# Optimization experiments

Hardware: AMD Instinct MI355X
Metric: run time of the kernel (lower is better)

Reference implementation:

```python
import jax, jax.numpy as jnp
import numpy as np

B = 131072
SD, AD, HID = 24, 8, 32
NH = SD + AD            # n_heads = 32
UNITS = HID * NH        # 1024


def _xavier(k, shape):
    fan_in, fan_out = shape[-2], shape[-1]
    lim = float(np.sqrt(6.0 / (fan_in + fan_out)))
    return jax.random.uniform(k, shape, jnp.float32, -lim, lim)


def setup_inputs() -> dict:
    key = jax.random.key(0)
    ks = jax.random.split(key, 8)
    return dict(
        state=jax.random.normal(ks[0], (B, SD), jnp.float32),
        action=jax.random.normal(ks[1], (B, AD), jnp.float32),
        # ripple layer 1: per-head Linear(NH -> HID), gate logits init 0 (init_prob=0.5)
        W1=_xavier(ks[2], (NH, NH, HID)), b1=jnp.zeros((NH, HID), jnp.float32), g1=jnp.zeros((NH,), jnp.float32),
        # ripple layer 2: per-head Linear(UNITS -> HID)
        W2=_xavier(ks[3], (NH, UNITS, HID)), b2=jnp.zeros((NH, HID), jnp.float32), g2=jnp.zeros((NH,), jnp.float32),
        # q_network
        Wq1=_xavier(ks[4], (UNITS, 256)), bq1=jnp.zeros((256,), jnp.float32),
        ln1_g=jnp.ones((256,), jnp.float32), ln1_b=jnp.zeros((256,), jnp.float32),
        Wq2=_xavier(ks[5], (256, 128)), bq2=jnp.zeros((128,), jnp.float32),
        ln2_g=jnp.ones((128,), jnp.float32), ln2_b=jnp.zeros((128,), jnp.float32),
        Wq3=_xavier(ks[6], (128, 1)), bq3=jnp.zeros((1,), jnp.float32),
    )


def _ripple(x, W, b, g):
    # x: [B, D]; W: [H, D, K]; per-head linear + tanh, scaled by per-head sigmoid gate
    h = jnp.tanh(jnp.einsum('bd,hdk->bhk', x, W) + b[None])  # [B, H, K]
    h = h * jax.nn.sigmoid(g)[None, :, None]
    return h.reshape(x.shape[0], -1)  # [B, H*K]


def _ln(x, g, b, eps=1e-5):
    mu = jnp.mean(x, -1, keepdims=True)
    var = jnp.mean((x - mu) ** 2, -1, keepdims=True)
    return (x - mu) * jax.lax.rsqrt(var + eps) * g + b


def reference(state, action, W1, b1, g1, W2, b2, g2,
              Wq1, bq1, ln1_g, ln1_b, Wq2, bq2, ln2_g, ln2_b, Wq3, bq3):
    sa = jnp.concatenate([state, action], axis=1)          # [B, SD+AD]
    x = _ripple(sa, W1, b1, g1)                            # [B, UNITS]
    x = _ripple(x, W2, b2, g2)                             # [B, UNITS]
    h = jax.nn.relu(_ln(x @ Wq1 + bq1, ln1_g, ln1_b))      # [B, 256] (dropout = eval identity)
    h = jax.nn.relu(_ln(h @ Wq2 + bq2, ln2_g, ln2_b))      # [B, 128]
    return h @ Wq3 + bq3                                   # [B, 1]
```

## Files before the change

kernel.cpp:

```cpp
#include <hip/hip_runtime.h>
#include <hip/hip_bf16.h>

typedef _Float16 f16x8 __attribute__((ext_vector_type(8)));
typedef float f32x4 __attribute__((ext_vector_type(4)));

__device__ __forceinline__ void async16(const _Float16* g, _Float16* l) {
  __builtin_amdgcn_global_load_lds(
      (const __attribute__((address_space(1))) unsigned int*)g,
      (__attribute__((address_space(3))) unsigned int*)l, 16, 0, 0);
}

__device__ __forceinline__ float tanh_fast(float x) {
  float e = __expf(2.0f * x);
  return 1.0f - 2.0f * __builtin_amdgcn_rcpf(e + 1.0f);
}
__device__ __forceinline__ float sigmoid_fast(float x) {
  return __builtin_amdgcn_rcpf(1.0f + __expf(-x));
}

__global__ __launch_bounds__(256) void transpose_cvt(const float* __restrict__ in,
                                                     _Float16* __restrict__ out,
                                                     int R, int C) {
  __shared__ float tile[32][33];
  int z = blockIdx.z;
  in  += (size_t)z * R * C;
  out += (size_t)z * R * C;
  int r0 = blockIdx.x * 32, c0 = blockIdx.y * 32;
  int t = threadIdx.x;
  int cc = t & 31, rr8 = t >> 5;
#pragma unroll
  for (int p = 0; p < 4; ++p) {
    int r = rr8 + p * 8;
    tile[cc][r] = in[(size_t)(r0 + r) * C + c0 + cc];
  }
  __syncthreads();
  int rr = t & 31, cc8 = t >> 5;
#pragma unroll
  for (int p = 0; p < 4; ++p) {
    int c = cc8 + p * 8;
    out[(size_t)(c0 + c) * R + r0 + rr] = (_Float16)tile[c][rr];
  }
}

__global__ __launch_bounds__(256) void k1_ripple1(
    const float* __restrict__ state, const float* __restrict__ action,
    const _Float16* __restrict__ v1t, const float* __restrict__ b1,
    const float* __restrict__ g1, _Float16* __restrict__ x1, int gro) {
  __shared__ __align__(16) _Float16 As[128 * 40];
  int bn = blockIdx.x, bm = blockIdx.y;
  int t = threadIdx.x, w = t >> 6, l = t & 63, q = l >> 4, l15 = l & 15;
  int n0 = bn * 128, m0 = bm * 128;

  {
    int r = t >> 1, half = t & 1;
    size_t grow = (size_t)(gro + m0 + r);
    float v[16];
    if (half == 0) {
      const float4* sp = (const float4*)(state + grow * 24);
      ((float4*)v)[0] = sp[0]; ((float4*)v)[1] = sp[1];
      ((float4*)v)[2] = sp[2]; ((float4*)v)[3] = sp[3];
    } else {
      const float4* sp = (const float4*)(state + grow * 24 + 16);
      ((float4*)v)[0] = sp[0]; ((float4*)v)[1] = sp[1];
      const float4* ap = (const float4*)(action + grow * 8);
      ((float4*)v)[2] = ap[0]; ((float4*)v)[3] = ap[1];
    }
    f16x8 h0, h1;
#pragma unroll
    for (int j = 0; j < 8; ++j) { h0[j] = (_Float16)v[j]; h1[j] = (_Float16)v[8 + j]; }
    *(f16x8*)&As[r * 40 + half * 16] = h0;
    *(f16x8*)&As[r * 40 + half * 16 + 8] = h1;
  }
  __syncthreads();

  int wr = w >> 1, wc = w & 1;
  f16x8 af[4], bf[4];
#pragma unroll
  for (int mi = 0; mi < 4; ++mi)
    af[mi] = *(const f16x8*)&As[(wr * 64 + mi * 16 + l15) * 40 + q * 8];
#pragma unroll
  for (int ni = 0; ni < 4; ++ni)
    bf[ni] = *(const f16x8*)(v1t + (size_t)(n0 + wc * 64 + ni * 16 + l15) * 32 + q * 8);

  f32x4 acc[4][4] = {};
#pragma unroll
  for (int mi = 0; mi < 4; ++mi)
#pragma unroll
    for (int ni = 0; ni < 4; ++ni)
      acc[mi][ni] = __builtin_amdgcn_mfma_f32_16x16x32_f16(af[mi], bf[ni], acc[mi][ni], 0, 0, 0);

#pragma unroll
  for (int ni = 0; ni < 4; ++ni) {
    int col = n0 + wc * 64 + ni * 16 + l15;
    float sg = sigmoid_fast(g1[col >> 5]);
    float bias = b1[col];
#pragma unroll
    for (int mi = 0; mi < 4; ++mi)
#pragma unroll
      for (int r = 0; r < 4; ++r) {
        int row = m0 + wr * 64 + mi * 16 + q * 4 + r;
        x1[(size_t)row * 1024 + col] = (_Float16)(tanh_fast(acc[mi][ni][r] + bias) * sg);
      }
  }
}

__global__ __launch_bounds__(256, 3) void k2_ripple2(
    const _Float16* __restrict__ x1, const _Float16* __restrict__ v2t,
    const float* __restrict__ b2, const float* __restrict__ g2,
    _Float16* __restrict__ x2, int nbm) {
  __shared__ __align__(16) _Float16 As[128 * 32];
  __shared__ __align__(16) _Float16 Bs[128 * 32];
  int g = blockIdx.x;
  int bn, bm;
  if ((nbm & 7) == 0) {
    int x = g & 7, j = g >> 3;
    bn = j & 7; bm = x + 8 * (j >> 3);
  } else { bn = g & 7; bm = g >> 3; }
  int t = threadIdx.x, w = t >> 6, l = t & 63, q = l >> 4, l15 = l & 15;
  int n0 = bn * 128, m0 = bm * 128;
  int wr = w >> 1, wc = w & 1;
  f32x4 acc[4][4] = {};

  int c0 = t, c1 = t + 256;
  const _Float16* aS0 = x1 + (size_t)(m0 + (c0 >> 2)) * 1024 + ((c0 & 3) ^ ((c0 >> 3) & 3)) * 8;
  const _Float16* aS1 = x1 + (size_t)(m0 + (c1 >> 2)) * 1024 + ((c1 & 3) ^ ((c1 >> 3) & 3)) * 8;
  const _Float16* bS0 = v2t + (size_t)(n0 + (c0 >> 2)) * 1024 + ((c0 & 3) ^ ((c0 >> 3) & 3)) * 8;
  const _Float16* bS1 = v2t + (size_t)(n0 + (c1 >> 2)) * 1024 + ((c1 & 3) ^ ((c1 >> 3) & 3)) * 8;
  _Float16* aD0 = As + c0 * 8; _Float16* aD1 = As + c1 * 8;
  _Float16* bD0 = Bs + c0 * 8; _Float16* bD1 = Bs + c1 * 8;
  int qs = q ^ ((l15 >> 1) & 3);

  for (int kt = 0; kt < 32; ++kt) {
    __syncthreads();
    int ko = kt * 32;
    async16(aS0 + ko, aD0);
    async16(aS1 + ko, aD1);
    async16(bS0 + ko, bD0);
    async16(bS1 + ko, bD1);
    __builtin_amdgcn_s_waitcnt(0);
    __syncthreads();
    f16x8 af[4], bf[4];
#pragma unroll
    for (int mi = 0; mi < 4; ++mi)
      af[mi] = *(const f16x8*)&As[(wr * 64 + mi * 16 + l15) * 32 + qs * 8];
#pragma unroll
    for (int ni = 0; ni < 4; ++ni)
      bf[ni] = *(const f16x8*)&Bs[(wc * 64 + ni * 16 + l15) * 32 + qs * 8];
#pragma unroll
    for (int mi = 0; mi < 4; ++mi)
#pragma unroll
      for (int ni = 0; ni < 4; ++ni)
        acc[mi][ni] = __builtin_amdgcn_mfma_f32_16x16x32_f16(af[mi], bf[ni], acc[mi][ni], 0, 0, 0);
  }

#pragma unroll
  for (int ni = 0; ni < 4; ++ni) {
    int col = n0 + wc * 64 + ni * 16 + l15;
    float sg = sigmoid_fast(g2[col >> 5]);
    float bias = b2[col];
#pragma unroll
    for (int mi = 0; mi < 4; ++mi)
#pragma unroll
      for (int r = 0; r < 4; ++r) {
        int row = m0 + wr * 64 + mi * 16 + q * 4 + r;
        x2[(size_t)row * 1024 + col] = (_Float16)(tanh_fast(acc[mi][ni][r] + bias) * sg);
      }
  }
}

__global__ __launch_bounds__(256) void k3_head(
    const _Float16* __restrict__ x2, const _Float16* __restrict__ t1t,
    const _Float16* __restrict__ t2t,
    const float* __restrict__ bq1, const float* __restrict__ ln1g, const float* __restrict__ ln1b,
    const float* __restrict__ bq2, const float* __restrict__ ln2g, const float* __restrict__ ln2b,
    const float* __restrict__ wq3, const float* __restrict__ bq3,
    float* __restrict__ out) {
  __shared__ __align__(16) _Float16 Ast[2 * 64 * 32];
  __shared__ __align__(16) _Float16 Bst[2 * 256 * 32];
  __shared__ __align__(16) _Float16 y1h[64 * 264];
  __shared__ float redA[64 * 4], redB[64 * 4];
  __shared__ float meanv[64], rstdv[64];
  int bm = blockIdx.x;
  int t = threadIdx.x, w = t >> 6, l = t & 63, q = l >> 4, l15 = l & 15;
  int m0 = bm * 64;
  int qs = q ^ ((l15 >> 1) & 3);

  f32x4 acc[4][4] = {};
  int cA = t;
  const _Float16* aS = x2 + (size_t)(m0 + (cA >> 2)) * 1024 + ((cA & 3) ^ ((cA >> 3) & 3)) * 8;
  _Float16* aD = Ast + cA * 8;
  const _Float16* bS[4]; _Float16* bD[4];
#pragma unroll
  for (int i = 0; i < 4; ++i) {
    int c = t + i * 256;
    bS[i] = t1t + (size_t)(c >> 2) * 1024 + ((c & 3) ^ ((c >> 3) & 3)) * 8;
    bD[i] = Bst + c * 8;
  }

  for (int kt = 0; kt < 16; ++kt) {
    __syncthreads();
    int ko = kt * 64;
    async16(aS + ko, aD);
    async16(aS + ko + 32, aD + 64 * 32);
#pragma unroll
    for (int i = 0; i < 4; ++i) {
      async16(bS[i] + ko, bD[i]);
      async16(bS[i] + ko + 32, bD[i] + 256 * 32);
    }
    __builtin_amdgcn_s_waitcnt(0);
    __syncthreads();
#pragma unroll
    for (int s = 0; s < 2; ++s) {
      f16x8 af[4], bf[4];
#pragma unroll
      for (int mi = 0; mi < 4; ++mi)
        af[mi] = *(const f16x8*)&Ast[s * 2048 + (mi * 16 + l15) * 32 + qs * 8];
#pragma unroll
      for (int ni = 0; ni < 4; ++ni)
        bf[ni] = *(const f16x8*)&Bst[s * 8192 + (w * 64 + ni * 16 + l15) * 32 + qs * 8];
#pragma unroll
      for (int mi = 0; mi < 4; ++mi)
#pragma unroll
        for (int ni = 0; ni < 4; ++ni)
          acc[mi][ni] = __builtin_amdgcn_mfma_f32_16x16x32_f16(af[mi], bf[ni], acc[mi][ni], 0, 0, 0);
    }
  }

#pragma unroll
  for (int ni = 0; ni < 4; ++ni) {
    int col = w * 64 + ni * 16 + l15;
    float b = bq1[col];
#pragma unroll
    for (int mi = 0; mi < 4; ++mi)
#pragma unroll
      for (int r = 0; r < 4; ++r) acc[mi][ni][r] += b;
  }
#pragma unroll
  for (int mi = 0; mi < 4; ++mi)
#pragma unroll
    for (int r = 0; r < 4; ++r) {
      int row = mi * 16 + q * 4 + r;
      float s = 0.f, sq = 0.f;
#pragma unroll
      for (int ni = 0; ni < 4; ++ni) { float v = acc[mi][ni][r]; s += v; sq += v * v; }
#pragma unroll
      for (int off = 1; off < 16; off <<= 1) { s += __shfl_xor(s, off); sq += __shfl_xor(sq, off); }
      if (l15 == 0) { redA[row * 4 + w] = s; redB[row * 4 + w] = sq; }
    }
  __syncthreads();
  if (t < 64) {
    float s  = redA[t * 4] + redA[t * 4 + 1] + redA[t * 4 + 2] + redA[t * 4 + 3];
    float sq = redB[t * 4] + redB[t * 4 + 1] + redB[t * 4 + 2] + redB[t * 4 + 3];
    float mean = s * (1.0f / 256.0f);
    float var = sq * (1.0f / 256.0f) - mean * mean;
    meanv[t] = mean; rstdv[t] = rsqrtf(var + 1e-5f);
  }
  __syncthreads();
#pragma unroll
  for (int mi = 0; mi < 4; ++mi)
#pragma unroll
    for (int ni = 0; ni < 4; ++ni)
#pragma unroll
      for (int r = 0; r < 4; ++r) {
        int row = mi * 16 + q * 4 + r;
        int col = w * 64 + ni * 16 + l15;
        float y = (acc[mi][ni][r] - meanv[row]) * rstdv[row] * ln1g[col] + ln1b[col];
        y = fmaxf(y, 0.f);
        y1h[row * 264 + col] = (_Float16)y;
      }
  __syncthreads();

  int wr = w >> 1, wc = w & 1;
  f32x4 a2[2][4] = {};
  for (int kt = 0; kt < 8; ++kt) {
    f16x8 af2[2];
#pragma unroll
    for (int mi = 0; mi < 2; ++mi)
      af2[mi] = *(const f16x8*)&y1h[(wr * 32 + mi * 16 + l15) * 264 + kt * 32 + q * 8];
#pragma unroll
    for (int ni = 0; ni < 4; ++ni) {
      f16x8 bf = *(const f16x8*)(t2t + (size_t)(wc * 64 + ni * 16 + l15) * 256 + kt * 32 + q * 8);
#pragma unroll
      for (int mi = 0; mi < 2; ++mi)
        a2[mi][ni] = __builtin_amdgcn_mfma_f32_16x16x32_f16(af2[mi], bf, a2[mi][ni], 0, 0, 0);
    }
  }
#pragma unroll
  for (int ni = 0; ni < 4; ++ni) {
    int col = wc * 64 + ni * 16 + l15;
    float b = bq2[col];
#pragma unroll
    for (int mi = 0; mi < 2; ++mi)
#pragma unroll
      for (int r = 0; r < 4; ++r) a2[mi][ni][r] += b;
  }
  __syncthreads();
#pragma unroll
  for (int mi = 0; mi < 2; ++mi)
#pragma unroll
    for (int r = 0; r < 4; ++r) {
      int row = wr * 32 + mi * 16 + q * 4 + r;
      float s = 0.f, sq = 0.f;
#pragma unroll
      for (int ni = 0; ni < 4; ++ni) { float v = a2[mi][ni][r]; s += v; sq += v * v; }
#pragma unroll
      for (int off = 1; off < 16; off <<= 1) { s += __shfl_xor(s, off); sq += __shfl_xor(sq, off); }
      if (l15 == 0) { redA[row * 2 + wc] = s; redB[row * 2 + wc] = sq; }
    }
  __syncthreads();
  if (t < 64) {
    float s = redA[t * 2] + redA[t * 2 + 1];
    float sq = redB[t * 2] + redB[t * 2 + 1];
    float mean = s * (1.0f / 128.0f);
    float var = sq * (1.0f / 128.0f) - mean * mean;
    meanv[t] = mean; rstdv[t] = rsqrtf(var + 1e-5f);
  }
  __syncthreads();
#pragma unroll
  for (int mi = 0; mi < 2; ++mi)
#pragma unroll
    for (int r = 0; r < 4; ++r) {
      int row = wr * 32 + mi * 16 + q * 4 + r;
      float pr = 0.f;
#pragma unroll
      for (int ni = 0; ni < 4; ++ni) {
        int col = wc * 64 + ni * 16 + l15;
        float y = (a2[mi][ni][r] - meanv[row]) * rstdv[row] * ln2g[col] + ln2b[col];
        y = fmaxf(y, 0.f);
        pr += y * wq3[col];
      }
#pragma unroll
      for (int off = 1; off < 16; off <<= 1) pr += __shfl_xor(pr, off);
      if (l15 == 0) redA[row * 2 + wc] = pr;
    }
  __syncthreads();
  if (t < 64) out[m0 + t] = redA[t * 2] + redA[t * 2 + 1] + bq3[0];
}

extern "C" void kernel_launch(void* const* d_in, const int* in_sizes, int n_in,
                              void* d_out, int out_size, void* d_ws, size_t ws_size,
                              hipStream_t stream) {
  const float* state  = (const float*)d_in[0];
  const float* action = (const float*)d_in[1];
  const float* W1  = (const float*)d_in[2];
  const float* b1  = (const float*)d_in[3];
  const float* g1  = (const float*)d_in[4];
  const float* W2  = (const float*)d_in[5];
  const float* b2  = (const float*)d_in[6];
  const float* g2  = (const float*)d_in[7];
  const float* Wq1 = (const float*)d_in[8];
  const float* bq1 = (const float*)d_in[9];
  const float* ln1g = (const float*)d_in[10];
  const float* ln1b = (const float*)d_in[11];
  const float* Wq2 = (const float*)d_in[12];
  const float* bq2 = (const float*)d_in[13];
  const float* ln2g = (const float*)d_in[14];
  const float* ln2b = (const float*)d_in[15];
  const float* Wq3 = (const float*)d_in[16];
  const float* bq3 = (const float*)d_in[17];
  int B = in_sizes[0] / 24;

  char* ws = (char*)d_ws;
  _Float16* V1t = (_Float16*)(ws);
  _Float16* V2t = (_Float16*)(ws + 65536);
  _Float16* T1t = (_Float16*)(ws + 65536 + 2097152);
  _Float16* T2t = (_Float16*)(ws + 65536 + 2097152 + 524288);
  size_t woff = (65536 + 2097152 + 524288 + 65536 + 4095) & ~(size_t)4095;

  size_t avail = ws_size > woff ? ws_size - woff : 0;
  long rows = (long)(avail / 4096);
  if (rows > 32768) rows = 32768;
  rows &= ~127L;
  if (rows < 128) rows = 128;
  int S = (int)rows;
  _Float16* x1 = (_Float16*)(ws + woff);
  _Float16* x2 = x1 + (size_t)S * 1024;

  transpose_cvt<<<dim3(1, 1, 32), 256, 0, stream>>>(W1, V1t, 32, 32);
  transpose_cvt<<<dim3(32, 1, 32), 256, 0, stream>>>(W2, V2t, 1024, 32);
  transpose_cvt<<<dim3(32, 8, 1), 256, 0, stream>>>(Wq1, T1t, 1024, 256);
  transpose_cvt<<<dim3(8, 4, 1), 256, 0, stream>>>(Wq2, T2t, 256, 128);

  for (int r0 = 0; r0 < B; r0 += S) {
    int Sc = S < (B - r0) ? S : (B - r0);
    int nbm = Sc / 128;
    k1_ripple1<<<dim3(8, nbm), 256, 0, stream>>>(state, action, V1t, b1, g1, x1, r0);
    k2_ripple2<<<dim3(8 * nbm), 256, 0, stream>>>(x1, V2t, b2, g2, x2, nbm);
    k3_head<<<dim3(Sc / 64), 256, 0, stream>>>(x2, T1t, T2t, bq1, ln1g, ln1b,
                                               bq2, ln2g, ln2b, Wq3, bq3,
                                               (float*)d_out + r0);
  }
}
```

Baseline: 702.6 us.

## Stage epilogue stores via LDS, merge weight transposes, retile head kernel

Merges the four weight-transpose launches into one kernel. The ripple epilogues now stage results in shared memory so global stores become coalesced 16-byte writes instead of scattered half-precision stores. The head kernel moves to 512 threads and 128-row tiles with a single-stage K loop, which halves how often the Wq1 tile is reloaded per row. When the workspace allows, k2 outputs are grouped so k3 launches over two slices at once. The trade-off is more LDS barriers in the epilogues and higher register and occupancy pressure in k3.

```diff
diff --git a/kernel.cpp b/kernel.cpp
--- a/kernel.cpp
+++ b/kernel.cpp
@@ -18,14 +18,26 @@
   return __builtin_amdgcn_rcpf(1.0f + __expf(-x));
 }
 
-__global__ __launch_bounds__(256) void transpose_cvt(const float* __restrict__ in,
-                                                     _Float16* __restrict__ out,
-                                                     int R, int C) {
+__global__ __launch_bounds__(256) void transpose_all(
+    const float* __restrict__ W1, const float* __restrict__ W2,
+    const float* __restrict__ Wq1, const float* __restrict__ Wq2,
+    _Float16* __restrict__ V1t, _Float16* __restrict__ V2t,
+    _Float16* __restrict__ T1t, _Float16* __restrict__ T2t) {
   __shared__ float tile[32][33];
-  int z = blockIdx.z;
-  in  += (size_t)z * R * C;
-  out += (size_t)z * R * C;
-  int r0 = blockIdx.x * 32, c0 = blockIdx.y * 32;
+  int b = blockIdx.x;
+  const float* in; _Float16* out; int R, C, rt, ct;
+  if (b < 32) {
+    in = W1 + b * 1024; out = V1t + b * 1024; R = 32; C = 32; rt = 0; ct = 0;
+  } else if (b < 32 + 1024) {
+    int i = b - 32; int z = i >> 5;
+    in = W2 + (size_t)z * 32768; out = V2t + (size_t)z * 32768;
+    R = 1024; C = 32; rt = i & 31; ct = 0;
+  } else if (b < 32 + 1024 + 256) {
+    int i = b - 1056; in = Wq1; out = T1t; R = 1024; C = 256; rt = i >> 3; ct = i & 7;
+  } else {
+    int i = b - 1312; in = Wq2; out = T2t; R = 256; C = 128; rt = i >> 2; ct = i & 3;
+  }
+  int r0 = rt * 32, c0 = ct * 32;
   int t = threadIdx.x;
   int cc = t & 31, rr8 = t >> 5;
 #pragma unroll
@@ -89,27 +101,37 @@
     for (int ni = 0; ni < 4; ++ni)
       acc[mi][ni] = __builtin_amdgcn_mfma_f32_16x16x32_f16(af[mi], bf[ni], acc[mi][ni], 0, 0, 0);
 
-#pragma unroll
   for (int ni = 0; ni < 4; ++ni) {
+    __syncthreads();
     int col = n0 + wc * 64 + ni * 16 + l15;
     float sg = sigmoid_fast(g1[col >> 5]);
     float bias = b1[col];
+    int cl = wc * 16 + l15;
 #pragma unroll
     for (int mi = 0; mi < 4; ++mi)
 #pragma unroll
       for (int r = 0; r < 4; ++r) {
-        int row = m0 + wr * 64 + mi * 16 + q * 4 + r;
-        x1[(size_t)row * 1024 + col] = (_Float16)(tanh_fast(acc[mi][ni][r] + bias) * sg);
+        int rl = wr * 64 + mi * 16 + q * 4 + r;
+        As[rl * 40 + cl] = (_Float16)(tanh_fast(acc[mi][ni][r] + bias) * sg);
       }
-  }
-}
-
-__global__ __launch_bounds__(256, 3) void k2_ripple2(
+    __syncthreads();
+#pragma unroll
+    for (int i = 0; i < 2; ++i) {
+      int c = t + i * 256;
+      int row = c >> 2, sub = c & 3;
+      int colg = n0 + (sub >> 1) * 64 + ni * 16 + (sub & 1) * 8;
+      *(float4*)(x1 + (size_t)(m0 + row) * 1024 + colg) = *(const float4*)&As[row * 40 + sub * 8];
+    }
+  }
+}
+
+__global__ __launch_bounds__(256, 4) void k2_ripple2(
     const _Float16* __restrict__ x1, const _Float16* __restrict__ v2t,
     const float* __restrict__ b2, const float* __restrict__ g2,
     _Float16* __restrict__ x2, int nbm) {
-  __shared__ __align__(16) _Float16 As[128 * 32];
-  __shared__ __align__(16) _Float16 Bs[128 * 32];
+  __shared__ __align__(16) _Float16 SMEM[9216];
+  _Float16* As = SMEM;
+  _Float16* Bs = SMEM + 4096;
   int g = blockIdx.x;
   int bn, bm;
   if ((nbm & 7) == 0) {
@@ -153,82 +175,86 @@
         acc[mi][ni] = __builtin_amdgcn_mfma_f32_16x16x32_f16(af[mi], bf[ni], acc[mi][ni], 0, 0, 0);
   }
 
-#pragma unroll
-  for (int ni = 0; ni < 4; ++ni) {
-    int col = n0 + wc * 64 + ni * 16 + l15;
-    float sg = sigmoid_fast(g2[col >> 5]);
-    float bias = b2[col];
-#pragma unroll
-    for (int mi = 0; mi < 4; ++mi)
-#pragma unroll
-      for (int r = 0; r < 4; ++r) {
-        int row = m0 + wr * 64 + mi * 16 + q * 4 + r;
-        x2[(size_t)row * 1024 + col] = (_Float16)(tanh_fast(acc[mi][ni][r] + bias) * sg);
-      }
-  }
-}
-
-__global__ __launch_bounds__(256) void k3_head(
+  for (int pass = 0; pass < 2; ++pass) {
+    __syncthreads();
+#pragma unroll
+    for (int ni2 = 0; ni2 < 2; ++ni2) {
+      int ni = pass * 2 + ni2;
+      int col = n0 + wc * 64 + ni * 16 + l15;
+      float sg = sigmoid_fast(g2[col >> 5]);
+      float bias = b2[col];
+      int cl = wc * 32 + ni2 * 16 + l15;
+#pragma unroll
+      for (int mi = 0; mi < 4; ++mi)
+#pragma unroll
+        for (int r = 0; r < 4; ++r) {
+          int rl = wr * 64 + mi * 16 + q * 4 + r;
+          SMEM[rl * 72 + cl] = (_Float16)(tanh_fast(acc[mi][ni][r] + bias) * sg);
+        }
+    }
+    __syncthreads();
+#pragma unroll
+    for (int i = 0; i < 4; ++i) {
+      int c = t + i * 256;
+      int row = c >> 3, sub = c & 7;
+      int colg = n0 + (sub >> 2) * 64 + (pass * 2 + ((sub >> 1) & 1)) * 16 + (sub & 1) * 8;
+      *(float4*)(x2 + (size_t)(m0 + row) * 1024 + colg) = *(const float4*)&SMEM[row * 72 + sub * 8];
+    }
+  }
+}
+
+__global__ __launch_bounds__(512, 4) void k3_head(
     const _Float16* __restrict__ x2, const _Float16* __restrict__ t1t,
     const _Float16* __restrict__ t2t,
     const float* __restrict__ bq1, const float* __restrict__ ln1g, const float* __restrict__ ln1b,
     const float* __restrict__ bq2, const float* __restrict__ ln2g, const float* __restrict__ ln2b,
     const float* __restrict__ wq3, const float* __restrict__ bq3,
     float* __restrict__ out) {
-  __shared__ __align__(16) _Float16 Ast[2 * 64 * 32];
-  __shared__ __align__(16) _Float16 Bst[2 * 256 * 32];
-  __shared__ __align__(16) _Float16 y1h[64 * 264];
-  __shared__ float redA[64 * 4], redB[64 * 4];
-  __shared__ float meanv[64], rstdv[64];
+  __shared__ __align__(16) _Float16 y1h[128 * 264];
+  __shared__ float redA[128 * 4], redB[128 * 4];
+  __shared__ float meanv[128], rstdv[128];
+  _Float16* Ast = y1h;
+  _Float16* Bst = y1h + 4096;
   int bm = blockIdx.x;
   int t = threadIdx.x, w = t >> 6, l = t & 63, q = l >> 4, l15 = l & 15;
-  int m0 = bm * 64;
+  int wr = w >> 2, wc = w & 3;
+  int m0 = bm * 128;
   int qs = q ^ ((l15 >> 1) & 3);
 
   f32x4 acc[4][4] = {};
-  int cA = t;
-  const _Float16* aS = x2 + (size_t)(m0 + (cA >> 2)) * 1024 + ((cA & 3) ^ ((cA >> 3) & 3)) * 8;
-  _Float16* aD = Ast + cA * 8;
-  const _Float16* bS[4]; _Float16* bD[4];
-#pragma unroll
-  for (int i = 0; i < 4; ++i) {
-    int c = t + i * 256;
-    bS[i] = t1t + (size_t)(c >> 2) * 1024 + ((c & 3) ^ ((c >> 3) & 3)) * 8;
-    bD[i] = Bst + c * 8;
-  }
-
-  for (int kt = 0; kt < 16; ++kt) {
-    __syncthreads();
-    int ko = kt * 64;
+  const _Float16* aS = x2 + (size_t)(m0 + (t >> 2)) * 1024 + ((t & 3) ^ ((t >> 3) & 3)) * 8;
+  _Float16* aD = Ast + t * 8;
+  int cb0 = t, cb1 = t + 512;
+  const _Float16* bS0 = t1t + (size_t)(cb0 >> 2) * 1024 + ((cb0 & 3) ^ ((cb0 >> 3) & 3)) * 8;
+  const _Float16* bS1 = t1t + (size_t)(cb1 >> 2) * 1024 + ((cb1 & 3) ^ ((cb1 >> 3) & 3)) * 8;
+  _Float16* bD0 = Bst + cb0 * 8;
+  _Float16* bD1 = Bst + cb1 * 8;
+
+  for (int kt = 0; kt < 32; ++kt) {
+    __syncthreads();
+    int ko = kt * 32;
     async16(aS + ko, aD);
-    async16(aS + ko + 32, aD + 64 * 32);
-#pragma unroll
-    for (int i = 0; i < 4; ++i) {
-      async16(bS[i] + ko, bD[i]);
-      async16(bS[i] + ko + 32, bD[i] + 256 * 32);
-    }
+    async16(bS0 + ko, bD0);
+    async16(bS1 + ko, bD1);
     __builtin_amdgcn_s_waitcnt(0);
     __syncthreads();
-#pragma unroll
-    for (int s = 0; s < 2; ++s) {
-      f16x8 af[4], bf[4];
-#pragma unroll
-      for (int mi = 0; mi < 4; ++mi)
-        af[mi] = *(const f16x8*)&Ast[s * 2048 + (mi * 16 + l15) * 32 + qs * 8];
+    f16x8 af[4], bf[4];
+#pragma unroll
+    for (int mi = 0; mi < 4; ++mi)
+      af[mi] = *(const f16x8*)&Ast[(wr * 64 + mi * 16 + l15) * 32 + qs * 8];
+#pragma unroll
+    for (int ni = 0; ni < 4; ++ni)
+      bf[ni] = *(const f16x8*)&Bst[(wc * 64 + ni * 16 + l15) * 32 + qs * 8];
+#pragma unroll
+    for (int mi = 0; mi < 4; ++mi)
 #pragma unroll
       for (int ni = 0; ni < 4; ++ni)
-        bf[ni] = *(const f16x8*)&Bst[s * 8192 + (w * 64 + ni * 16 + l15) * 32 + qs * 8];
-#pragma unroll
-      for (int mi = 0; mi < 4; ++mi)
-#pragma unroll
-        for (int ni = 0; ni < 4; ++ni)
-          acc[mi][ni] = __builtin_amdgcn_mfma_f32_16x16x32_f16(af[mi], bf[ni], acc[mi][ni], 0, 0, 0);
-    }
+        acc[mi][ni] = __builtin_amdgcn_mfma_f32_16x16x32_f16(af[mi], bf[ni], acc[mi][ni], 0, 0, 0);
   }
 
 #pragma unroll
   for (int ni = 0; ni < 4; ++ni) {
-    int col = w * 64 + ni * 16 + l15;
+    int col = wc * 64 + ni * 16 + l15;
     float b = bq1[col];
 #pragma unroll
     for (int mi = 0; mi < 4; ++mi)
@@ -239,16 +265,16 @@
   for (int mi = 0; mi < 4; ++mi)
 #pragma unroll
     for (int r = 0; r < 4; ++r) {
-      int row = mi * 16 + q * 4 + r;
+      int row = wr * 64 + mi * 16 + q * 4 + r;
       float s = 0.f, sq = 0.f;
 #pragma unroll
       for (int ni = 0; ni < 4; ++ni) { float v = acc[mi][ni][r]; s += v; sq += v * v; }
 #pragma unroll
       for (int off = 1; off < 16; off <<= 1) { s += __shfl_xor(s, off); sq += __shfl_xor(sq, off); }
-      if (l15 == 0) { redA[row * 4 + w] = s; redB[row * 4 + w] = sq; }
-    }
-  __syncthreads();
-  if (t < 64) {
+      if (l15 == 0) { redA[row * 4 + wc] = s; redB[row * 4 + wc] = sq; }
+    }
+  __syncthreads();
+  if (t < 128) {
     float s  = redA[t * 4] + redA[t * 4 + 1] + redA[t * 4 + 2] + redA[t * 4 + 3];
     float sq = redB[t * 4] + redB[t * 4 + 1] + redB[t * 4 + 2] + redB[t * 4 + 3];
     float mean = s * (1.0f / 256.0f);
@@ -262,79 +288,79 @@
     for (int ni = 0; ni < 4; ++ni)
 #pragma unroll
       for (int r = 0; r < 4; ++r) {
-        int row = mi * 16 + q * 4 + r;
-        int col = w * 64 + ni * 16 + l15;
+        int row = wr * 64 + mi * 16 + q * 4 + r;
+        int col = wc * 64 + ni * 16 + l15;
         float y = (acc[mi][ni][r] - meanv[row]) * rstdv[row] * ln1g[col] + ln1b[col];
         y = fmaxf(y, 0.f);
         y1h[row * 264 + col] = (_Float16)y;
       }
   __syncthreads();
 
-  int wr = w >> 1, wc = w & 1;
-  f32x4 a2[2][4] = {};
+  f32x4 a2[4][2] = {};
   for (int kt = 0; kt < 8; ++kt) {
-    f16x8 af2[2];
-#pragma unroll
-    for (int mi = 0; mi < 2; ++mi)
-      af2[mi] = *(const f16x8*)&y1h[(wr * 32 + mi * 16 + l15) * 264 + kt * 32 + q * 8];
-#pragma unroll
-    for (int ni = 0; ni < 4; ++ni) {
-      f16x8 bf = *(const f16x8*)(t2t + (size_t)(wc * 64 + ni * 16 + l15) * 256 + kt * 32 + q * 8);
-#pragma unroll
-      for (int mi = 0; mi < 2; ++mi)
+    f16x8 af2[4];
+#pragma unroll
+    for (int mi = 0; mi < 4; ++mi)
+      af2[mi] = *(const f16x8*)&y1h[(wr * 64 + mi * 16 + l15) * 264 + kt * 32 + q * 8];
+#pragma unroll
+    for (int ni = 0; ni < 2; ++ni) {
+      f16x8 bf = *(const f16x8*)(t2t + (size_t)(wc * 32 + ni * 16 + l15) * 256 + kt * 32 + q * 8);
+#pragma unroll
+      for (int mi = 0; mi < 4; ++mi)
         a2[mi][ni] = __builtin_amdgcn_mfma_f32_16x16x32_f16(af2[mi], bf, a2[mi][ni], 0, 0, 0);
     }
   }
 #pragma unroll
-  for (int ni = 0; ni < 4; ++ni) {
-    int col = wc * 64 + ni * 16 + l15;
+  for (int ni = 0; ni < 2; ++ni) {
+    int col = wc * 32 + ni * 16 + l15;
     float b = bq2[col];
 #pragma unroll
-    for (int mi = 0; mi < 2; ++mi)
+    for (int mi = 0; mi < 4; ++mi)
 #pragma unroll
       for (int r = 0; r < 4; ++r) a2[mi][ni][r] += b;
   }
   __syncthreads();
 #pragma unroll
-  for (int mi = 0; mi < 2; ++mi)
+  for (int mi = 0; mi < 4; ++mi)
 #pragma unroll
     for (int r = 0; r < 4; ++r) {
-      int row = wr * 32 + mi * 16 + q * 4 + r;
+      int row = wr * 64 + mi * 16 + q * 4 + r;
       float s = 0.f, sq = 0.f;
 #pragma unroll
-      for (int ni = 0; ni < 4; ++ni) { float v = a2[mi][ni][r]; s += v; sq += v * v; }
+      for (int ni = 0; ni < 2; ++ni) { float v = a2[mi][ni][r]; s += v; sq += v * v; }
 #pragma unroll
       for (int off = 1; off < 16; off <<= 1) { s += __shfl_xor(s, off); sq += __shfl_xor(sq, off); }
-      if (l15 == 0) { redA[row * 2 + wc] = s; redB[row * 2 + wc] = sq; }
-    }
-  __syncthreads();
-  if (t < 64) {
-    float s = redA[t * 2] + redA[t * 2 + 1];
-    float sq = redB[t * 2] + redB[t * 2 + 1];
+      if (l15 == 0) { redA[row * 4 + wc] = s; redB[row * 4 + wc] = sq; }
+    }
+  __syncthreads();
+  if (t < 128) {
+    float s  = redA[t * 4] + redA[t * 4 + 1] + redA[t * 4 + 2] + redA[t * 4 + 3];
+    float sq = redB[t * 4] + redB[t * 4 + 1] + redB[t * 4 + 2] + redB[t * 4 + 3];
     float mean = s * (1.0f / 128.0f);
     float var = sq * (1.0f / 128.0f) - mean * mean;
     meanv[t] = mean; rstdv[t] = rsqrtf(var + 1e-5f);
   }
   __syncthreads();
 #pragma unroll
-  for (int mi = 0; mi < 2; ++mi)
+  for (int mi = 0; mi < 4; ++mi)
 #pragma unroll
     for (int r = 0; r < 4; ++r) {
-      int row = wr * 32 + mi * 16 + q * 4 + r;
+      int row = wr * 64 + mi * 16 + q * 4 + r;
       float pr = 0.f;
 #pragma unroll
-      for (int ni = 0; ni < 4; ++ni) {
-        int col = wc * 64 + ni * 16 + l15;
+      for (int ni = 0; ni < 2; ++ni) {
+        int col = wc * 32 + ni * 16 + l15;
         float y = (a2[mi][ni][r] - meanv[row]) * rstdv[row] * ln2g[col] + ln2b[col];
         y = fmaxf(y, 0.f);
         pr += y * wq3[col];
       }
 #pragma unroll
       for (int off = 1; off < 16; off <<= 1) pr += __shfl_xor(pr, off);
-      if (l15 == 0) redA[row * 2 + wc] = pr;
-    }
-  __syncthreads();
-  if (t < 64) out[m0 + t] = redA[t * 2] + redA[t * 2 + 1] + bq3[0];
+      if (l15 == 0) redA[row * 4 + wc] = pr;
+    }
+  __syncthreads();
+  if (t < 128)
+    out[m0 + t] = redA[t * 4] + redA[t * 4 + 1] + redA[t * 4 + 2] + redA[t * 4 + 3] + bq3[0];
 }
 
 extern "C" void kernel_launch(void* const* d_in, const int* in_sizes, int n_in,
@@ -368,26 +394,35 @@
   size_t woff = (65536 + 2097152 + 524288 + 65536 + 4095) & ~(size_t)4095;
 
   size_t avail = ws_size > woff ? ws_size - woff : 0;
-  long rows = (long)(avail / 4096);
-  if (rows > 32768) rows = 32768;
-  rows &= ~127L;
-  if (rows < 128) rows = 128;
-  int S = (int)rows;
+  int S, G;
+  if (avail >= (size_t)32768 * 2048 * 3) {
+    S = 32768; G = 2;
+  } else {
+    long rows = (long)(avail / 4096);
+    if (rows > 32768) rows = 32768;
+    rows &= ~127L;
+    if (rows < 128) rows = 128;
+    S = (int)rows; G = 1;
+  }
   _Float16* x1 = (_Float16*)(ws + woff);
   _Float16* x2 = x1 + (size_t)S * 1024;
 
-  transpose_cvt<<<dim3(1, 1, 32), 256, 0, stream>>>(W1, V1t, 32, 32);
-  transpose_cvt<<<dim3(32, 1, 32), 256, 0, stream>>>(W2, V2t, 1024, 32);
-  transpose_cvt<<<dim3(32, 8, 1), 256, 0, stream>>>(Wq1, T1t, 1024, 256);
-  transpose_cvt<<<dim3(8, 4, 1), 256, 0, stream>>>(Wq2, T2t, 256, 128);
-
-  for (int r0 = 0; r0 < B; r0 += S) {
+  transpose_all<<<1344, 256, 0, stream>>>(W1, W2, Wq1, Wq2, V1t, V2t, T1t, T2t);
+
+  int nsl = (B + S - 1) / S;
+  for (int i = 0; i < nsl; ++i) {
+    int r0 = i * S;
     int Sc = S < (B - r0) ? S : (B - r0);
     int nbm = Sc / 128;
     k1_ripple1<<<dim3(8, nbm), 256, 0, stream>>>(state, action, V1t, b1, g1, x1, r0);
-    k2_ripple2<<<dim3(8 * nbm), 256, 0, stream>>>(x1, V2t, b2, g2, x2, nbm);
-    k3_head<<<dim3(Sc / 64), 256, 0, stream>>>(x2, T1t, T2t, bq1, ln1g, ln1b,
-                                               bq2, ln2g, ln2b, Wq3, bq3,
-                                               (float*)d_out + r0);
-  }
-}
+    k2_ripple2<<<dim3(8 * nbm), 256, 0, stream>>>(x1, V2t, b2, g2,
+                                                  x2 + (size_t)(i % G) * S * 1024, nbm);
+    if (i % G == G - 1 || i == nsl - 1) {
+      int gstart = (i - i % G) * S;
+      int nrows = r0 + Sc - gstart;
+      k3_head<<<dim3(nrows / 128), 512, 0, stream>>>(x2, T1t, T2t, bq1, ln1g, ln1b,
+                                                     bq2, ln2g, ln2b, Wq3, bq3,
+                                                     (float*)d_out + gstart);
+    }
+  }
+}
```

Result: no change. 694.4 us (-1.2%).
